# Kernel tuning notes

Hardware: AMD Instinct MI355X
Metric: run time of the kernel (lower is better)

The kernel has to match this reference:

```python
import jax, jax.numpy as jnp
import numpy as np

HIDDEN = 4096
NUM_HEADS = 32
NUM_KV_HEADS = 8
HEAD_DIM = 128
EPS = 1e-6
ROPE_THETA = 1000000.0
T = 2048


def setup_inputs() -> dict:
    key = jax.random.key(0)
    k1, k2, k3, k4, k5 = jax.random.split(key, 5)
    q_size = NUM_HEADS * HEAD_DIM
    kv_size = NUM_KV_HEADS * HEAD_DIM
    return {
        "positions": jnp.arange(T, dtype=jnp.int32),
        "hidden_states": jax.random.normal(k1, (T, HIDDEN), dtype=jnp.float32),
        "w_qkv": jax.random.normal(k2, (HIDDEN, q_size + 2 * kv_size), dtype=jnp.float32) * 0.02,
        "w_o": jax.random.normal(k3, (q_size, HIDDEN), dtype=jnp.float32) * 0.02,
        "q_norm_w": jnp.ones((HEAD_DIM,), dtype=jnp.float32) + 0.01 * jax.random.normal(k4, (HEAD_DIM,), dtype=jnp.float32),
        "k_norm_w": jnp.ones((HEAD_DIM,), dtype=jnp.float32) + 0.01 * jax.random.normal(k5, (HEAD_DIM,), dtype=jnp.float32),
    }


def _rms_norm(x, w, eps=EPS):
    # x: [..., head_dim], normalize over last dim
    var = jnp.mean(jnp.square(x), axis=-1, keepdims=True)
    return x * jax.lax.rsqrt(var + eps) * w


def _apply_rope(x, positions):
    # neox-style rotate-half RoPE, rotary_dim == head_dim
    d = x.shape[-1]
    inv_freq = 1.0 / (ROPE_THETA ** (jnp.arange(0, d, 2, dtype=jnp.float32) / d))
    freqs = positions.astype(jnp.float32)[:, None] * inv_freq[None, :]  # [T, d/2]
    cos = jnp.cos(freqs)[:, None, :]  # [T, 1, d/2]
    sin = jnp.sin(freqs)[:, None, :]
    x1, x2 = jnp.split(x, 2, axis=-1)
    return jnp.concatenate([x1 * cos - x2 * sin, x2 * cos + x1 * sin], axis=-1)


def reference(positions, hidden_states, w_qkv, w_o, q_norm_w, k_norm_w):
    num_tokens = hidden_states.shape[0]
    q_size = NUM_HEADS * HEAD_DIM
    kv_size = NUM_KV_HEADS * HEAD_DIM
    group = NUM_HEADS // NUM_KV_HEADS

    qkv = hidden_states @ w_qkv  # [T, q+2kv]
    q = qkv[:, :q_size].reshape(num_tokens, NUM_HEADS, HEAD_DIM)
    k = qkv[:, q_size:q_size + kv_size].reshape(num_tokens, NUM_KV_HEADS, HEAD_DIM)
    v = qkv[:, q_size + kv_size:].reshape(num_tokens, NUM_KV_HEADS, HEAD_DIM)

    q = _rms_norm(q, q_norm_w)
    k = _rms_norm(k, k_norm_w)
    q = _apply_rope(q, positions)
    k = _apply_rope(k, positions)

    scale = HEAD_DIM ** -0.5
    # GQA: group query heads over shared kv heads
    qg = q.reshape(num_tokens, NUM_KV_HEADS, group, HEAD_DIM)
    scores = jnp.einsum("tkgd,skd->kgts", qg * scale, k)  # [KH, G, T, S]
    causal = positions[:, None] >= positions[None, :]  # [T, S]
    scores = jnp.where(causal[None, None, :, :], scores, jnp.finfo(scores.dtype).min)
    probs = jax.nn.softmax(scores, axis=-1)
    out = jnp.einsum("kgts,skd->tkgd", probs, v)  # [T, KH, G, D]
    out = out.reshape(num_tokens, q_size)
    return out @ w_o
```

## Files before the change

### kernel.cpp

```cpp
#include <hip/hip_runtime.h>
#include <cstdint>
#include <cstddef>

#define T_TOK 2048
#define HID   4096
#define NQH   32
#define NKVH  8
#define HD    128
#define QKV_N 6144

typedef __bf16 bf16x8 __attribute__((ext_vector_type(8)));
typedef __bf16 bf16x4 __attribute__((ext_vector_type(4)));
typedef float  f32x4  __attribute__((ext_vector_type(4)));
typedef float  f32x16 __attribute__((ext_vector_type(16)));

#define AS1 __attribute__((address_space(1)))
#define AS3 __attribute__((address_space(3)))

__device__ __forceinline__ void gll16(const void* g, void* l) {
  __builtin_amdgcn_global_load_lds((const AS1 void*)g, (AS3 void*)l, 16, 0, 0);
}

__global__ __launch_bounds__(256) void k_convert(const float* __restrict__ in,
                                                 __bf16* __restrict__ out, int n4) {
  int i = blockIdx.x * 256 + threadIdx.x;
  if (i >= n4) return;
  float4 v = ((const float4*)in)[i];
  bf16x4 o;
  o[0] = (__bf16)v.x; o[1] = (__bf16)v.y; o[2] = (__bf16)v.z; o[3] = (__bf16)v.w;
  ((bf16x4*)out)[i] = o;
}

__global__ __launch_bounds__(256) void k_transpose(const float* __restrict__ in,
                                                   __bf16* __restrict__ out,
                                                   int R, int C) {
  __shared__ float tile[64][33];
  const int tid = threadIdx.x;
  const int c0 = blockIdx.x * 32, r0 = blockIdx.y * 64;
  const int ty = tid >> 3, tx = tid & 7;
#pragma unroll
  for (int k = 0; k < 2; ++k) {
    float4 v = *(const float4*)&in[(size_t)(r0 + ty + k * 32) * C + c0 + tx * 4];
    tile[ty + k * 32][tx * 4 + 0] = v.x;
    tile[ty + k * 32][tx * 4 + 1] = v.y;
    tile[ty + k * 32][tx * 4 + 2] = v.z;
    tile[ty + k * 32][tx * 4 + 3] = v.w;
  }
  __syncthreads();
  const int c = tid >> 3, rq = tid & 7;
  bf16x8 o;
#pragma unroll
  for (int i = 0; i < 8; ++i) o[i] = (__bf16)tile[rq * 8 + i][c];
  *(bf16x8*)&out[(size_t)(c0 + c) * R + r0 + rq * 8] = o;
}

__global__ __launch_bounds__(256) void k_vtrans(const float* __restrict__ qkv,
                                                __bf16* __restrict__ vt) {
  __shared__ float tile[64][33];
  const int tid = threadIdx.x;
  const int kvh = blockIdx.z;
  const int d0 = blockIdx.x * 32;
  const int t0 = blockIdx.y * 64;
  const int ty = tid >> 3, tx = tid & 7;
#pragma unroll
  for (int k = 0; k < 2; ++k) {
    float4 v = *(const float4*)&qkv[(size_t)(t0 + ty + k * 32) * QKV_N + 5120 + kvh * 128 + d0 + tx * 4];
    tile[ty + k * 32][tx * 4 + 0] = v.x;
    tile[ty + k * 32][tx * 4 + 1] = v.y;
    tile[ty + k * 32][tx * 4 + 2] = v.z;
    tile[ty + k * 32][tx * 4 + 3] = v.w;
  }
  __syncthreads();
  const int d = tid >> 3, tq = tid & 7;
  bf16x8 o;
#pragma unroll
  for (int i = 0; i < 8; ++i) o[i] = (__bf16)tile[tq * 8 + i][d];
  *(bf16x8*)&vt[((size_t)kvh * 128 + d0 + d) * T_TOK + t0 + tq * 8] = o;
}

template <int NFR>
__global__ __launch_bounds__(512, 2) void k_gemm8(const __bf16* __restrict__ A,
                                                  const __bf16* __restrict__ Bt,
                                                  float* __restrict__ C,
                                                  int N, int K) {
  constexpr int BN   = 64 * NFR;
  constexpr int WN   = 16 * NFR;
  constexpr int NB   = NFR / 2;
  constexpr int NH   = NFR / 2;
  constexpr int BREG = BN * 64;
  constexpr int BUFSZ = 16384 + 2 * BREG;
  __shared__ alignas(16) char ldsb[2 * BUFSZ];
  const int tid = threadIdx.x;
  const int lane = tid & 63, w = tid >> 6;
  const int l16 = lane & 15, lg = lane >> 4;
  const int wm = w >> 2, wn = w & 3;

  const int x = blockIdx.x & 7, idx = blockIdx.x >> 3;
  const int bm = (x & 1) * 8 + (idx & 7);
  const int bn = (x >> 1) * 4 + (idx >> 3);

  const int rA = tid >> 2, pA = tid & 3;
  const __bf16* asrc = A + (size_t)(bm * 128 + rA) * K + ((pA ^ ((rA >> 1) & 3)) * 8);
  const __bf16* bsrc = Bt + (size_t)(bn * BN + rA) * K + ((pA ^ ((rA >> 1) & 3)) * 8);

#define RA_(buf, mk) (ldsb + (buf) * BUFSZ + (mk) * 8192)
#define RB_(buf, mk) (ldsb + (buf) * BUFSZ + 16384 + (mk) * BREG)
#define STG_A(buf, mk, kk) { gll16(asrc + (kk) + (mk) * 32, RA_(buf, mk) + w * 1024); }
#define STG_B(buf, mk, kk) { _Pragma("unroll") \
    for (int j = 0; j < NB; ++j) \
      gll16(bsrc + (size_t)j * 128 * K + (kk) + (mk) * 32, RB_(buf, mk) + j * 8192 + w * 1024); }
#define FRAG(base, row) (*(const bf16x8*)((base) + (row) * 64 + ((lg ^ (((row) >> 1) & 3)) << 4)))
#define WAITN() { if constexpr (NFR == 6) asm volatile("s_waitcnt vmcnt(4)" ::: "memory"); \
                  else                    asm volatile("s_waitcnt vmcnt(3)" ::: "memory"); }

  f32x4 acc[4][NFR] = {};
  const int nkt = K >> 6;

  STG_A(0, 0, 0); STG_B(0, 0, 0); STG_A(0, 1, 0); STG_B(0, 1, 0);

  for (int t = 0; t < nkt - 1; ++t) {
    const int cur = t & 1, nxt = cur ^ 1;
    const int kn = (t + 1) * 64;
    bf16x8 af[4], bf_[NH];

    STG_A(nxt, 0, kn);
    WAITN();
    __builtin_amdgcn_s_barrier();
    __builtin_amdgcn_sched_barrier(0);
#pragma unroll
    for (int i = 0; i < 4; ++i) af[i] = FRAG(RA_(cur, 0), wm * 64 + i * 16 + l16);
#pragma unroll
    for (int n = 0; n < NH; ++n) bf_[n] = FRAG(RB_(cur, 0), wn * WN + n * 16 + l16);
    __builtin_amdgcn_s_setprio(1);
#pragma unroll
    for (int i = 0; i < 4; ++i)
#pragma unroll
      for (int n = 0; n < NH; ++n)
        acc[i][n] = __builtin_amdgcn_mfma_f32_16x16x32_bf16(af[i], bf_[n], acc[i][n], 0, 0, 0);
    __builtin_amdgcn_s_setprio(0);
    __builtin_amdgcn_s_barrier();

#pragma unroll
    for (int n = 0; n < NH; ++n) bf_[n] = FRAG(RB_(cur, 0), wn * WN + (NH + n) * 16 + l16);
    STG_B(nxt, 0, kn);
    __builtin_amdgcn_s_barrier();
    __builtin_amdgcn_s_setprio(1);
#pragma unroll
    for (int i = 0; i < 4; ++i)
#pragma unroll
      for (int n = 0; n < NH; ++n)
        acc[i][NH + n] = __builtin_amdgcn_mfma_f32_16x16x32_bf16(af[i], bf_[n], acc[i][NH + n], 0, 0, 0);
    __builtin_amdgcn_s_setprio(0);
    __builtin_amdgcn_s_barrier();

    STG_A(nxt, 1, kn);
    WAITN();
    __builtin_amdgcn_s_barrier();
    __builtin_amdgcn_sched_barrier(0);
#pragma unroll
    for (int i = 0; i < 4; ++i) af[i] = FRAG(RA_(cur, 1), wm * 64 + i * 16 + l16);
#pragma unroll
    for (int n = 0; n < NH; ++n) bf_[n] = FRAG(RB_(cur, 1), wn * WN + n * 16 + l16);
    __builtin_amdgcn_s_setprio(1);
#pragma unroll
    for (int i = 0; i < 4; ++i)
#pragma unroll
      for (int n = 0; n < NH; ++n)
        acc[i][n] = __builtin_amdgcn_mfma_f32_16x16x32_bf16(af[i], bf_[n], acc[i][n], 0, 0, 0);
    __builtin_amdgcn_s_setprio(0);
    __builtin_amdgcn_s_barrier();

#pragma unroll
    for (int n = 0; n < NH; ++n) bf_[n] = FRAG(RB_(cur, 1), wn * WN + (NH + n) * 16 + l16);
    STG_B(nxt, 1, kn);
    __builtin_amdgcn_s_barrier();
    __builtin_amdgcn_s_setprio(1);
#pragma unroll
    for (int i = 0; i < 4; ++i)
#pragma unroll
      for (int n = 0; n < NH; ++n)
        acc[i][NH + n] = __builtin_amdgcn_mfma_f32_16x16x32_bf16(af[i], bf_[n], acc[i][NH + n], 0, 0, 0);
    __builtin_amdgcn_s_setprio(0);
    __builtin_amdgcn_s_barrier();
  }

  asm volatile("s_waitcnt vmcnt(0)" ::: "memory");
  __builtin_amdgcn_s_barrier();
  __builtin_amdgcn_sched_barrier(0);
  {
    const int cur = (nkt - 1) & 1;
#pragma unroll
    for (int mk = 0; mk < 2; ++mk) {
      bf16x8 aa[4], bb[NFR];
#pragma unroll
      for (int i = 0; i < 4; ++i) aa[i] = FRAG(RA_(cur, mk), wm * 64 + i * 16 + l16);
#pragma unroll
      for (int n = 0; n < NFR; ++n) bb[n] = FRAG(RB_(cur, mk), wn * WN + n * 16 + l16);
#pragma unroll
      for (int i = 0; i < 4; ++i)
#pragma unroll
        for (int n = 0; n < NFR; ++n)
          acc[i][n] = __builtin_amdgcn_mfma_f32_16x16x32_bf16(aa[i], bb[n], acc[i][n], 0, 0, 0);
    }
  }
#undef RA_
#undef RB_
#undef STG_A
#undef STG_B
#undef FRAG
#undef WAITN

#pragma unroll
  for (int mi = 0; mi < 4; ++mi)
#pragma unroll
    for (int ni = 0; ni < NFR; ++ni) {
      int row = bm * 128 + wm * 64 + mi * 16 + lg * 4;
      int col = bn * BN + wn * WN + ni * 16 + l16;
#pragma unroll
      for (int r = 0; r < 4; ++r)
        C[(size_t)(row + r) * N + col] = acc[mi][ni][r];
    }
}

__global__ __launch_bounds__(256) void k_norm_rope(const float* __restrict__ qkv,
                                                   const int* __restrict__ pos,
                                                   const float* __restrict__ qw,
                                                   const float* __restrict__ kw,
                                                   __bf16* __restrict__ qo,
                                                   __bf16* __restrict__ ko) {
  const int t = blockIdx.x;
  const int w = threadIdx.x >> 6, i = threadIdx.x & 63;
  const float fr = (float)pos[t] * expf((float)i * -0.21586735246819178f);
  const float cs = cosf(fr), sn = sinf(fr);
  const float qwi1 = qw[i], qwi2 = qw[i + 64];
  const float kwi1 = kw[i], kwi2 = kw[i + 64];
  const float* base = qkv + (size_t)t * QKV_N;
#pragma unroll
  for (int s = 0; s < 10; ++s) {
    const int slot = w * 10 + s;
    const int off = (slot < 32) ? slot * 128 : 4096 + (slot - 32) * 128;
    float x1 = base[off + i], x2 = base[off + i + 64];
    float ss = x1 * x1 + x2 * x2;
#pragma unroll
    for (int m = 32; m >= 1; m >>= 1) ss += __shfl_xor(ss, m);
    float rinv = rsqrtf(ss * (1.0f / 128.0f) + 1e-6f);
    float n1, n2;
    if (slot < 32) { n1 = x1 * rinv * qwi1; n2 = x2 * rinv * qwi2; }
    else           { n1 = x1 * rinv * kwi1; n2 = x2 * rinv * kwi2; }
    float o1 = n1 * cs - n2 * sn;
    float o2 = n2 * cs + n1 * sn;
    if (slot < 32) {
      const float QSC = 0.08838834764831845f * 1.4426950408889634f;
      __bf16* o = qo + ((size_t)t * NQH + slot) * HD;
      o[i] = (__bf16)(o1 * QSC);
      o[i + 64] = (__bf16)(o2 * QSC);
    } else {
      __bf16* o = ko + ((size_t)t * NKVH + (slot - 32)) * HD;
      o[i] = (__bf16)o1;
      o[i + 64] = (__bf16)o2;
    }
  }
}

__global__ __launch_bounds__(256, 2) void k_attn(const __bf16* __restrict__ Q,
                                                 const __bf16* __restrict__ K,
                                                 const __bf16* __restrict__ Vt,
                                                 __bf16* __restrict__ O) {
  __shared__ alignas(16) __bf16 Ks[64 * 128];
  __shared__ alignas(16) __bf16 Vts[128 * 64];
  const int bid = blockIdx.x;
  const int kvh = bid & 7;
  const int qc  = bid >> 3;
  const int tid = threadIdx.x, lane = tid & 63, w = tid >> 6;
  const int l31 = lane & 31, hi = lane >> 5;
  const int h  = kvh * 4 + w;
  const int q0 = qc * 32;
  const int qrow = q0 + l31;
  char* Ksb = (char*)Ks;
  char* Vtb = (char*)Vts;

  bf16x8 qf[8];
  {
    const __bf16* qp = Q + ((size_t)qrow * NQH + h) * HD + hi * 8;
#pragma unroll
    for (int dc = 0; dc < 8; ++dc)
      qf[dc] = *(const bf16x8*)(qp + dc * 16);
  }

  size_t ksrc[4], vsrc[4];
#pragma unroll
  for (int j = 0; j < 4; ++j) {
    int kr = w * 16 + j * 4 + (lane >> 4);
    ksrc[j] = ((size_t)kr * NKVH + kvh) * HD + (size_t)(((lane & 15) ^ (kr & 15)) * 8);
    int vr = w * 32 + j * 8 + (lane >> 3);
    vsrc[j] = ((size_t)(kvh * HD + vr)) * T_TOK + (size_t)(((lane & 7) ^ (vr & 7)) * 8);
  }

  float m_run = -3.0e38f, l_run = 0.f;
  f32x16 ot[4] = {};

  const int ntiles = (qc >> 1) + 1;
  for (int tt = 0; tt < ntiles; ++tt) {
    const int s0 = tt * 64;
#pragma unroll
    for (int j = 0; j < 4; ++j) {
      gll16(K + (size_t)s0 * (NKVH * HD) + ksrc[j], Ksb + (w * 4 + j) * 1024);
      gll16(Vt + (size_t)s0 + vsrc[j], Vtb + (w * 4 + j) * 1024);
    }
    __syncthreads();

    f32x16 sac[2] = {};
#pragma unroll
    for (int hf = 0; hf < 2; ++hf) {
      int krow = hf * 32 + l31;
#pragma unroll
      for (int dc = 0; dc < 8; ++dc) {
        bf16x8 kf = *(const bf16x8*)(Ksb + krow * 256 + (((dc * 2 + hi) ^ (krow & 15)) * 16));
        sac[hf] = __builtin_amdgcn_mfma_f32_32x32x16_bf16(kf, qf[dc], sac[hf], 0, 0, 0);
      }
    }

    float pv[32];
    if (s0 + 64 > q0) {
#pragma unroll
      for (int hf = 0; hf < 2; ++hf)
#pragma unroll
        for (int r = 0; r < 16; ++r) {
          int kvg = s0 + hf * 32 + (r & 3) + ((r >> 2) * 8) + hi * 4;
          pv[hf * 16 + r] = (kvg > qrow) ? -3.0e38f : sac[hf][r];
        }
    } else {
#pragma unroll
      for (int hf = 0; hf < 2; ++hf)
#pragma unroll
        for (int r = 0; r < 16; ++r) pv[hf * 16 + r] = sac[hf][r];
    }
    float t16[16];
#pragma unroll
    for (int i = 0; i < 16; ++i) t16[i] = fmaxf(pv[i], pv[i + 16]);
#pragma unroll
    for (int i = 0; i < 8; ++i) t16[i] = fmaxf(t16[i], t16[i + 8]);
#pragma unroll
    for (int i = 0; i < 4; ++i) t16[i] = fmaxf(t16[i], t16[i + 4]);
    float mt = fmaxf(fmaxf(t16[0], t16[1]), fmaxf(t16[2], t16[3]));
    mt = fmaxf(mt, __shfl_xor(mt, 32));
    if (!__all(mt - m_run <= 10.0f)) {
      float m_new = fmaxf(m_run, mt);
      float corr = exp2f(m_run - m_new);
      l_run *= corr;
#pragma unroll
      for (int dt = 0; dt < 4; ++dt)
#pragma unroll
        for (int r = 0; r < 16; ++r) ot[dt][r] *= corr;
      m_run = m_new;
    }
#pragma unroll
    for (int i = 0; i < 32; ++i) pv[i] = exp2f(pv[i] - m_run);
#pragma unroll
    for (int i = 0; i < 16; ++i) t16[i] = pv[i] + pv[i + 16];
#pragma unroll
    for (int i = 0; i < 8; ++i) t16[i] += t16[i + 8];
#pragma unroll
    for (int i = 0; i < 4; ++i) t16[i] += t16[i + 4];
    float rs = (t16[0] + t16[1]) + (t16[2] + t16[3]);
    rs += __shfl_xor(rs, 32);
    l_run += rs;

    uint32_t wds[16];
#pragma unroll
    for (int i = 0; i < 16; ++i) {
      uint32_t r;
      asm("v_cvt_pk_bf16_f32 %0, %1, %2" : "=v"(r) : "v"(pv[2 * i]), "v"(pv[2 * i + 1]));
      wds[i] = r;
    }
#pragma unroll
    for (int c = 0; c < 4; ++c) {
      const int base = (c >> 1) * 8 + (c & 1) * 4;
      uint32_t sa = hi ? wds[base + 0] : wds[base + 2];
      uint32_t sb = hi ? wds[base + 1] : wds[base + 3];
      uint32_t ra = __shfl_xor(sa, 32);
      uint32_t rb = __shfl_xor(sb, 32);
      union { uint32_t u[4]; bf16x8 v; } pf;
      pf.u[0] = hi ? ra : wds[base + 0];
      pf.u[1] = hi ? rb : wds[base + 1];
      pf.u[2] = hi ? wds[base + 2] : ra;
      pf.u[3] = hi ? wds[base + 3] : rb;
#pragma unroll
      for (int dt = 0; dt < 4; ++dt) {
        int vrow = dt * 32 + l31;
        bf16x8 vf = *(const bf16x8*)(Vtb + vrow * 128 + (((c * 2 + hi) ^ (vrow & 7)) * 16));
        ot[dt] = __builtin_amdgcn_mfma_f32_32x32x16_bf16(vf, pf.v, ot[dt], 0, 0, 0);
      }
    }
    __syncthreads();
  }

  float inv = 1.0f / l_run;
  char* Ob = Ksb + w * 8192;
#pragma unroll
  for (int dt = 0; dt < 4; ++dt)
#pragma unroll
    for (int r = 0; r < 16; ++r) {
      int d = dt * 32 + (r & 3) + ((r >> 2) * 8) + hi * 4;
      *(__bf16*)(Ob + l31 * 256 + ((d * 2) ^ ((l31 & 7) << 4))) = (__bf16)(ot[dt][r] * inv);
    }
#pragma unroll
  for (int pass = 0; pass < 8; ++pass) {
    int q = pass * 4 + (lane >> 4);
    int ch = lane & 15;
    bf16x8 vvv = *(const bf16x8*)(Ob + q * 256 + ((ch ^ (q & 7)) * 16));
    *(bf16x8*)(O + ((size_t)(q0 + q) * NQH + h) * HD + ch * 8) = vvv;
  }
}

extern "C" void kernel_launch(void* const* d_in, const int* in_sizes, int n_in,
                              void* d_out, int out_size, void* d_ws, size_t ws_size,
                              hipStream_t stream) {
  const int*   positions = (const int*)d_in[0];
  const float* hidden    = (const float*)d_in[1];
  const float* w_qkv     = (const float*)d_in[2];
  const float* w_o       = (const float*)d_in[3];
  const float* q_norm    = (const float*)d_in[4];
  const float* k_norm    = (const float*)d_in[5];
  float* out = (float*)d_out;

  char* ws = (char*)d_ws;
  __bf16* wqkv_t   = (__bf16*)ws;
  __bf16* wo_t     = (__bf16*)(ws + 50331648);
  __bf16* hidden_b = (__bf16*)(ws + 83886080);
  float*  qkv      = (float*)(ws + 100663296);
  __bf16* qb  = (__bf16*)ws;
  __bf16* kb  = (__bf16*)(ws + 16777216);
  __bf16* vtb = (__bf16*)(ws + 20971520);
  __bf16* attn_o = hidden_b;

  k_convert<<<dim3((T_TOK * HID / 4 + 255) / 256), 256, 0, stream>>>(hidden, hidden_b, T_TOK * HID / 4);
  k_transpose<<<dim3(QKV_N / 32, HID / 64), 256, 0, stream>>>(w_qkv, wqkv_t, HID, QKV_N);
  k_transpose<<<dim3(HID / 32, HID / 64), 256, 0, stream>>>(w_o, wo_t, HID, HID);
  k_gemm8<6><<<dim3(256), 512, 0, stream>>>(hidden_b, wqkv_t, qkv, QKV_N, HID);
  k_norm_rope<<<dim3(T_TOK), 256, 0, stream>>>(qkv, positions, q_norm, k_norm, qb, kb);
  k_vtrans<<<dim3(4, T_TOK / 64, NKVH), 256, 0, stream>>>(qkv, vtb);
  k_attn<<<dim3(512), 256, 0, stream>>>(qb, kb, vtb, attn_o);
  k_gemm8<4><<<dim3(256), 512, 0, stream>>>(attn_o, wo_t, out, HID, HID);
}
```

Before: 319.0 us.

## Store QKV in bf16, widen transpose tiles, add 64-row GEMM for output projection

The QKV projection GEMM now writes bf16 instead of fp32, which halves the intermediate traffic read by norm/rope and the V transpose. The transpose kernels now use 64x64 tiles so each block does more work. A new 256-thread GEMM kernel with 64-row tiles and 512 blocks replaces the 512-thread kernel for the output projection, to give more blocks and better occupancy. Rounding QKV to bf16 before the RMS norm adds some precision loss.

New measurement: 337.5 us. 5.8% more time.

```diff
diff --git a/kernel.cpp b/kernel.cpp
--- a/kernel.cpp
+++ b/kernel.cpp
@@ -34,54 +34,58 @@
 __global__ __launch_bounds__(256) void k_transpose(const float* __restrict__ in,
                                                    __bf16* __restrict__ out,
                                                    int R, int C) {
-  __shared__ float tile[64][33];
+  __shared__ float tile[64][65];
   const int tid = threadIdx.x;
-  const int c0 = blockIdx.x * 32, r0 = blockIdx.y * 64;
-  const int ty = tid >> 3, tx = tid & 7;
-#pragma unroll
-  for (int k = 0; k < 2; ++k) {
-    float4 v = *(const float4*)&in[(size_t)(r0 + ty + k * 32) * C + c0 + tx * 4];
-    tile[ty + k * 32][tx * 4 + 0] = v.x;
-    tile[ty + k * 32][tx * 4 + 1] = v.y;
-    tile[ty + k * 32][tx * 4 + 2] = v.z;
-    tile[ty + k * 32][tx * 4 + 3] = v.w;
+  const int c0 = blockIdx.x * 64, r0 = blockIdx.y * 64;
+  const int ty = tid >> 4, tx = tid & 15;
+#pragma unroll
+  for (int k = 0; k < 4; ++k) {
+    float4 v = *(const float4*)&in[(size_t)(r0 + ty + k * 16) * C + c0 + tx * 4];
+    tile[ty + k * 16][tx * 4 + 0] = v.x;
+    tile[ty + k * 16][tx * 4 + 1] = v.y;
+    tile[ty + k * 16][tx * 4 + 2] = v.z;
+    tile[ty + k * 16][tx * 4 + 3] = v.w;
   }
   __syncthreads();
-  const int c = tid >> 3, rq = tid & 7;
-  bf16x8 o;
-#pragma unroll
-  for (int i = 0; i < 8; ++i) o[i] = (__bf16)tile[rq * 8 + i][c];
-  *(bf16x8*)&out[(size_t)(c0 + c) * R + r0 + rq * 8] = o;
-}
-
-__global__ __launch_bounds__(256) void k_vtrans(const float* __restrict__ qkv,
+  const int c = tid >> 2, rq = tid & 3;
+#pragma unroll
+  for (int h = 0; h < 2; ++h) {
+    bf16x8 o;
+#pragma unroll
+    for (int i = 0; i < 8; ++i) o[i] = (__bf16)tile[rq * 16 + h * 8 + i][c];
+    *(bf16x8*)&out[(size_t)(c0 + c) * R + r0 + rq * 16 + h * 8] = o;
+  }
+}
+
+__global__ __launch_bounds__(256) void k_vtrans(const __bf16* __restrict__ qkv,
                                                 __bf16* __restrict__ vt) {
-  __shared__ float tile[64][33];
+  __shared__ float tile[64][65];
   const int tid = threadIdx.x;
   const int kvh = blockIdx.z;
-  const int d0 = blockIdx.x * 32;
+  const int d0 = blockIdx.x * 64;
   const int t0 = blockIdx.y * 64;
-  const int ty = tid >> 3, tx = tid & 7;
-#pragma unroll
-  for (int k = 0; k < 2; ++k) {
-    float4 v = *(const float4*)&qkv[(size_t)(t0 + ty + k * 32) * QKV_N + 5120 + kvh * 128 + d0 + tx * 4];
-    tile[ty + k * 32][tx * 4 + 0] = v.x;
-    tile[ty + k * 32][tx * 4 + 1] = v.y;
-    tile[ty + k * 32][tx * 4 + 2] = v.z;
-    tile[ty + k * 32][tx * 4 + 3] = v.w;
+  const int ty = tid >> 4, tx = tid & 15;
+#pragma unroll
+  for (int k = 0; k < 4; ++k) {
+    bf16x4 v = *(const bf16x4*)&qkv[(size_t)(t0 + ty + k * 16) * QKV_N + 5120 + kvh * 128 + d0 + tx * 4];
+#pragma unroll
+    for (int j = 0; j < 4; ++j) tile[ty + k * 16][tx * 4 + j] = (float)v[j];
   }
   __syncthreads();
-  const int d = tid >> 3, tq = tid & 7;
-  bf16x8 o;
-#pragma unroll
-  for (int i = 0; i < 8; ++i) o[i] = (__bf16)tile[tq * 8 + i][d];
-  *(bf16x8*)&vt[((size_t)kvh * 128 + d0 + d) * T_TOK + t0 + tq * 8] = o;
-}
-
-template <int NFR>
+  const int d = tid >> 2, tq = tid & 3;
+#pragma unroll
+  for (int h = 0; h < 2; ++h) {
+    bf16x8 o;
+#pragma unroll
+    for (int i = 0; i < 8; ++i) o[i] = (__bf16)tile[tq * 16 + h * 8 + i][d];
+    *(bf16x8*)&vt[((size_t)kvh * 128 + d0 + d) * T_TOK + t0 + tq * 16 + h * 8] = o;
+  }
+}
+
+template <int NFR, typename OUT>
 __global__ __launch_bounds__(512, 2) void k_gemm8(const __bf16* __restrict__ A,
                                                   const __bf16* __restrict__ Bt,
-                                                  float* __restrict__ C,
+                                                  OUT* __restrict__ C,
                                                   int N, int K) {
   constexpr int BN   = 64 * NFR;
   constexpr int WN   = 16 * NFR;
@@ -218,11 +222,101 @@
       int col = bn * BN + wn * WN + ni * 16 + l16;
 #pragma unroll
       for (int r = 0; r < 4; ++r)
-        C[(size_t)(row + r) * N + col] = acc[mi][ni][r];
-    }
-}
-
-__global__ __launch_bounds__(256) void k_norm_rope(const float* __restrict__ qkv,
+        C[(size_t)(row + r) * N + col] = (OUT)acc[mi][ni][r];
+    }
+}
+
+template <int NFR, typename OUT>
+__global__ __launch_bounds__(256, 2) void k_g32(const __bf16* __restrict__ A,
+                                                const __bf16* __restrict__ Bt,
+                                                OUT* __restrict__ C,
+                                                int N, int K) {
+  constexpr int BN   = 64 * NFR;
+  constexpr int WN   = 16 * NFR;
+  constexpr int BREG = BN * 64;
+  constexpr int BUFSZ = 4096 + BREG;
+  __shared__ alignas(16) char ldsb[2 * BUFSZ];
+  const int tid = threadIdx.x;
+  const int lane = tid & 63, w = tid >> 6;
+  const int l16 = lane & 15, lg = lane >> 4;
+
+  const int x = blockIdx.x & 7, idx = blockIdx.x >> 3;
+  const int bm = (x & 3) * 8 + (idx & 7);
+  const int bn = (x >> 2) * 8 + (idx >> 3);
+
+  const int rS = tid >> 2, pS = tid & 3;
+  const int sw = (pS ^ ((rS >> 1) & 3)) * 8;
+  const __bf16* asrc = A + (size_t)(bm * 64 + rS) * K + sw;
+  const __bf16* bsrc = Bt + (size_t)(bn * BN + rS) * K + sw;
+
+#define RA_(buf) (ldsb + (buf) * BUFSZ)
+#define RB_(buf) (ldsb + (buf) * BUFSZ + 4096)
+#define STG(buf, kk) { gll16(asrc + (kk), RA_(buf) + tid * 16); \
+    _Pragma("unroll") for (int j = 0; j < NFR; ++j) \
+      gll16(bsrc + (size_t)j * 64 * K + (kk), RB_(buf) + j * 4096 + tid * 16); }
+#define FRAG(base, row) (*(const bf16x8*)((base) + (row) * 64 + ((lg ^ (((row) >> 1) & 3)) << 4)))
+#define WAITN() { if constexpr (NFR == 6) asm volatile("s_waitcnt vmcnt(7)" ::: "memory"); \
+                  else                    asm volatile("s_waitcnt vmcnt(5)" ::: "memory"); }
+
+  f32x4 acc[4][NFR] = {};
+  const int nkt = K >> 5;
+
+  STG(0, 0);
+  for (int t = 0; t < nkt - 1; ++t) {
+    const int cur = t & 1, nxt = cur ^ 1;
+    STG(nxt, (t + 1) * 32);
+    WAITN();
+    __builtin_amdgcn_s_barrier();
+    __builtin_amdgcn_sched_barrier(0);
+    bf16x8 af[4], bf_[NFR];
+#pragma unroll
+    for (int i = 0; i < 4; ++i) af[i] = FRAG(RA_(cur), i * 16 + l16);
+#pragma unroll
+    for (int n = 0; n < NFR; ++n) bf_[n] = FRAG(RB_(cur), w * WN + n * 16 + l16);
+    __builtin_amdgcn_s_setprio(1);
+#pragma unroll
+    for (int i = 0; i < 4; ++i)
+#pragma unroll
+      for (int n = 0; n < NFR; ++n)
+        acc[i][n] = __builtin_amdgcn_mfma_f32_16x16x32_bf16(af[i], bf_[n], acc[i][n], 0, 0, 0);
+    __builtin_amdgcn_s_setprio(0);
+    __builtin_amdgcn_s_barrier();
+  }
+  asm volatile("s_waitcnt vmcnt(0)" ::: "memory");
+  __builtin_amdgcn_s_barrier();
+  __builtin_amdgcn_sched_barrier(0);
+  {
+    const int cur = (nkt - 1) & 1;
+    bf16x8 af[4], bf_[NFR];
+#pragma unroll
+    for (int i = 0; i < 4; ++i) af[i] = FRAG(RA_(cur), i * 16 + l16);
+#pragma unroll
+    for (int n = 0; n < NFR; ++n) bf_[n] = FRAG(RB_(cur), w * WN + n * 16 + l16);
+#pragma unroll
+    for (int i = 0; i < 4; ++i)
+#pragma unroll
+      for (int n = 0; n < NFR; ++n)
+        acc[i][n] = __builtin_amdgcn_mfma_f32_16x16x32_bf16(af[i], bf_[n], acc[i][n], 0, 0, 0);
+  }
+#undef RA_
+#undef RB_
+#undef STG
+#undef FRAG
+#undef WAITN
+
+#pragma unroll
+  for (int mi = 0; mi < 4; ++mi)
+#pragma unroll
+    for (int ni = 0; ni < NFR; ++ni) {
+      int row = bm * 64 + mi * 16 + lg * 4;
+      int col = bn * BN + w * WN + ni * 16 + l16;
+#pragma unroll
+      for (int r = 0; r < 4; ++r)
+        C[(size_t)(row + r) * N + col] = (OUT)acc[mi][ni][r];
+    }
+}
+
+__global__ __launch_bounds__(256) void k_norm_rope(const __bf16* __restrict__ qkv,
                                                    const int* __restrict__ pos,
                                                    const float* __restrict__ qw,
                                                    const float* __restrict__ kw,
@@ -234,12 +328,12 @@
   const float cs = cosf(fr), sn = sinf(fr);
   const float qwi1 = qw[i], qwi2 = qw[i + 64];
   const float kwi1 = kw[i], kwi2 = kw[i + 64];
-  const float* base = qkv + (size_t)t * QKV_N;
+  const __bf16* base = qkv + (size_t)t * QKV_N;
 #pragma unroll
   for (int s = 0; s < 10; ++s) {
     const int slot = w * 10 + s;
     const int off = (slot < 32) ? slot * 128 : 4096 + (slot - 32) * 128;
-    float x1 = base[off + i], x2 = base[off + i + 64];
+    float x1 = (float)base[off + i], x2 = (float)base[off + i + 64];
     float ss = x1 * x1 + x2 * x2;
 #pragma unroll
     for (int m = 32; m >= 1; m >>= 1) ss += __shfl_xor(ss, m);
@@ -428,18 +522,18 @@
   __bf16* wqkv_t   = (__bf16*)ws;
   __bf16* wo_t     = (__bf16*)(ws + 50331648);
   __bf16* hidden_b = (__bf16*)(ws + 83886080);
-  float*  qkv      = (float*)(ws + 100663296);
+  __bf16* qkvb     = (__bf16*)(ws + 100663296);
   __bf16* qb  = (__bf16*)ws;
   __bf16* kb  = (__bf16*)(ws + 16777216);
   __bf16* vtb = (__bf16*)(ws + 20971520);
   __bf16* attn_o = hidden_b;
 
   k_convert<<<dim3((T_TOK * HID / 4 + 255) / 256), 256, 0, stream>>>(hidden, hidden_b, T_TOK * HID / 4);
-  k_transpose<<<dim3(QKV_N / 32, HID / 64), 256, 0, stream>>>(w_qkv, wqkv_t, HID, QKV_N);
-  k_transpose<<<dim3(HID / 32, HID / 64), 256, 0, stream>>>(w_o, wo_t, HID, HID);
-  k_gemm8<6><<<dim3(256), 512, 0, stream>>>(hidden_b, wqkv_t, qkv, QKV_N, HID);
-  k_norm_rope<<<dim3(T_TOK), 256, 0, stream>>>(qkv, positions, q_norm, k_norm, qb, kb);
-  k_vtrans<<<dim3(4, T_TOK / 64, NKVH), 256, 0, stream>>>(qkv, vtb);
+  k_transpose<<<dim3(QKV_N / 64, HID / 64), 256, 0, stream>>>(w_qkv, wqkv_t, HID, QKV_N);
+  k_transpose<<<dim3(HID / 64, HID / 64), 256, 0, stream>>>(w_o, wo_t, HID, HID);
+  k_gemm8<6, __bf16><<<dim3(256), 512, 0, stream>>>(hidden_b, wqkv_t, qkvb, QKV_N, HID);
+  k_norm_rope<<<dim3(T_TOK), 256, 0, stream>>>(qkvb, positions, q_norm, k_norm, qb, kb);
+  k_vtrans<<<dim3(2, T_TOK / 64, NKVH), 256, 0, stream>>>(qkvb, vtb);
   k_attn<<<dim3(512), 256, 0, stream>>>(qb, kb, vtb, attn_o);
-  k_gemm8<4><<<dim3(256), 512, 0, stream>>>(attn_o, wo_t, out, HID, HID);
-}
+  k_g32<4, float><<<dim3(512), 256, 0, stream>>>(attn_o, wo_t, out, HID, HID);
+}
```
